# Optimization experiments

Measured on AMD Instinct MI355X. Metric: run time of the kernel, lower is better.

## Reference

```python
import jax, jax.numpy as jnp
import numpy as np

N, D = 8192, 128
BATCH_SIZE = 8192  # init kwarg; final loss divisor
EPS = 1e-12        # F.normalize eps


def _normalize(x):
    n = jnp.maximum(jnp.linalg.norm(x, axis=-1, keepdims=True), EPS)
    return x / n


def _alignment(x, y, alpha=2.0):
    # (x - y).norm(p=2, dim=1).pow(2).mean() == mean of squared row diffs
    return jnp.mean(jnp.sum((x - y) ** 2, axis=1))


def _uniformity(x, t=2.0):
    # torch.pdist(x).pow(2) == squared euclidean distance for all i<j pairs.
    # Use gram-matrix identity; mask to strict upper triangle.
    n = x.shape[0]
    sq = jnp.sum(x * x, axis=1)                      # [N]
    d2 = sq[:, None] + sq[None, :] - 2.0 * (x @ x.T)  # [N, N]
    d2 = jnp.maximum(d2, 0.0)
    iu = jnp.triu(jnp.ones((n, n), dtype=bool), k=1)
    num_pairs = n * (n - 1) // 2
    mean_val = jnp.sum(jnp.where(iu, jnp.exp(-t * d2), 0.0)) / num_pairs
    return jnp.log(mean_val)


def setup_inputs() -> dict:
    key = jax.random.key(0)
    k1, k2, k3 = jax.random.split(key, 3)
    return {
        "users": jax.random.normal(k1, (N, D), dtype=jnp.float32),
        "pos_items": jax.random.normal(k2, (N, D), dtype=jnp.float32),
        "neg_items": jax.random.normal(k3, (N, D), dtype=jnp.float32),
    }


def reference(users, pos_items, neg_items):
    # neg_items is accepted but unused, matching the original forward.
    user_n = _normalize(users)
    item_n = _normalize(pos_items)
    align = _alignment(user_n, item_n)
    uniform = 0.5 * (_uniformity(user_n) + _uniformity(item_n)) / 2.0
    loss = (align + uniform) / BATCH_SIZE
    return loss
```

## Files before the change

### kernel.cpp

```cpp
#include <hip/hip_runtime.h>
#include <hip/hip_bf16.h>

typedef int   i32x4  __attribute__((ext_vector_type(4)));
typedef int   i32x16 __attribute__((ext_vector_type(16)));

#define NROWS 8192
#define DIM   128
#define NB    64
#define JOBS_PER_MAT 2080

__device__ __forceinline__ float waveReduceSum(float v) {
    for (int off = 32; off; off >>= 1) v += __shfl_xor(v, off, 64);
    return v;
}

__device__ __forceinline__ float fast_exp2(float x) {
    return __builtin_amdgcn_exp2f(x);
}

__device__ __forceinline__ void gload16(const void* g, void* l) {
    __builtin_amdgcn_global_load_lds(
        (const __attribute__((address_space(1))) unsigned int*)(uintptr_t)g,
        (__attribute__((address_space(3))) unsigned int*)(uintptr_t)l,
        16, 0, 0);
}

__device__ __forceinline__ int tri(int b) { return b * NB - (b * (b - 1)) / 2; }

__global__ __launch_bounds__(256) void prep_kernel(
    const float* __restrict__ users, const float* __restrict__ pos,
    signed char* __restrict__ U8, signed char* __restrict__ P8,
    double* __restrict__ alignPart)
{
    const int tid  = threadIdx.x;
    const int lane = tid & 63;
    const int w    = tid >> 6;
    const int l32  = lane & 31;
    const int half = lane >> 5;
    const int r    = blockIdx.x * 8 + w * 2 + half;

    const float4 u4 = ((const float4*)users)[r * 32 + l32];
    const float4 p4 = ((const float4*)pos )[r * 32 + l32];

    float su = u4.x*u4.x + u4.y*u4.y + u4.z*u4.z + u4.w*u4.w;
    float sp = p4.x*p4.x + p4.y*p4.y + p4.z*p4.z + p4.w*p4.w;
    for (int off = 16; off; off >>= 1) {
        su += __shfl_xor(su, off, 64);
        sp += __shfl_xor(sp, off, 64);
    }
    const float nu  = fmaxf(sqrtf(su), 1e-12f);
    const float npp = fmaxf(sqrtf(sp), 1e-12f);

    const float ux = u4.x / nu,  uy = u4.y / nu,  uz = u4.z / nu,  uw = u4.w / nu;
    const float px = p4.x / npp, py = p4.y / npp, pz = p4.z / npp, pw = p4.w / npp;

    union { signed char c[4]; int i; } qu, qp;
    qu.c[0] = (signed char)__float2int_rn(ux * 127.0f);
    qu.c[1] = (signed char)__float2int_rn(uy * 127.0f);
    qu.c[2] = (signed char)__float2int_rn(uz * 127.0f);
    qu.c[3] = (signed char)__float2int_rn(uw * 127.0f);
    qp.c[0] = (signed char)__float2int_rn(px * 127.0f);
    qp.c[1] = (signed char)__float2int_rn(py * 127.0f);
    qp.c[2] = (signed char)__float2int_rn(pz * 127.0f);
    qp.c[3] = (signed char)__float2int_rn(pw * 127.0f);
    ((int*)U8)[r * 32 + l32] = qu.i;
    ((int*)P8)[r * 32 + l32] = qp.i;

    const float dx = ux - px, dy = uy - py, dz = uz - pz, dw = uw - pw;
    float al = dx*dx + dy*dy + dz*dz + dw*dw;
    for (int off = 16; off; off >>= 1) al += __shfl_xor(al, off, 64);
    al += __shfl_xor(al, 32, 64);

    __shared__ float wsum[4];
    if (lane == 0) wsum[w] = al;
    __syncthreads();
    if (tid == 0)
        alignPart[blockIdx.x] = (double)wsum[0] + (double)wsum[1]
                              + (double)wsum[2] + (double)wsum[3];
}

__global__ __launch_bounds__(256, 4) void gram_kernel(
    const signed char* __restrict__ U8, const signed char* __restrict__ P8,
    double* __restrict__ Spart)
{
    __shared__ __align__(16) unsigned char smem[32768];
    __shared__ float wsum[4];

    const int bid = blockIdx.x;
    const int mat = bid >= JOBS_PER_MAT;
    const int t   = bid - (mat ? JOBS_PER_MAT : 0);

    int bi = (int)((NB + 0.5f) - sqrtf((NB + 0.5f) * (NB + 0.5f) - 2.0f * (float)t));
    if (bi > 0 && tri(bi) > t) --bi;
    if (tri(bi + 1) <= t) ++bi;
    const int bj = bi + (t - tri(bi));

    const char* __restrict__ Xb = (const char*)(mat ? P8 : U8);

    const int tid  = threadIdx.x;
    const int lane = tid & 63;
    const int w    = tid >> 6;

    const int srow = tid >> 3;
    const int gcOff = (((tid & 7) ^ (srow & 7)) << 4);
    const char* gA0 = Xb + (size_t)(bi * 128 + srow) * 128 + gcOff;
    const char* gB0 = Xb + (size_t)(bj * 128 + srow) * 128 + gcOff;
    unsigned char* lA0 = smem + w * 1024;

#pragma unroll
    for (int i = 0; i < 4; ++i) {
        gload16(gA0 + i * 4096, lA0 + i * 4096);
        gload16(gB0 + i * 4096, lA0 + 16384 + i * 4096);
    }

    const int wm = w >> 1, wn = w & 1;
    const int l32 = lane & 31;
    const int lh  = lane >> 5;
    const unsigned cxor = (unsigned)(l32 & 7);
    const unsigned aRow0 = (unsigned)(wm * 64 + l32);
    const unsigned bRow0 = (unsigned)(wn * 64 + l32);

    i32x16 acc[2][2];
#pragma unroll
    for (int mi = 0; mi < 2; ++mi)
#pragma unroll
        for (int ni = 0; ni < 2; ++ni)
#pragma unroll
            for (int e = 0; e < 16; ++e)
                acc[mi][ni][e] = 0;

    __syncthreads();

#pragma unroll
    for (int ks = 0; ks < 4; ++ks) {
        const unsigned c = (((unsigned)(ks * 2 + lh)) ^ cxor) << 4;
        i32x4 a[2], b[2];
#pragma unroll
        for (int mi = 0; mi < 2; ++mi)
            a[mi] = *reinterpret_cast<const i32x4*>(
                smem + (aRow0 + mi * 32) * 128 + c);
#pragma unroll
        for (int ni = 0; ni < 2; ++ni)
            b[ni] = *reinterpret_cast<const i32x4*>(
                smem + 16384 + (bRow0 + ni * 32) * 128 + c);
#pragma unroll
        for (int mi = 0; mi < 2; ++mi)
#pragma unroll
            for (int ni = 0; ni < 2; ++ni)
                acc[mi][ni] = __builtin_amdgcn_mfma_i32_32x32x32_i8(
                    a[mi], b[ni], acc[mi][ni], 0, 0, 0);
    }

    const float C1  = 4.0f * 1.4426950408889634f;
    const float C1s = C1 / 16129.0f;
    float s0 = 0.f, s1 = 0.f, s2 = 0.f, s3 = 0.f;
#pragma unroll
    for (int mi = 0; mi < 2; ++mi)
#pragma unroll
        for (int ni = 0; ni < 2; ++ni) {
            const i32x16 v = acc[mi][ni];
#pragma unroll
            for (int e = 0; e < 16; e += 4) {
                s0 += fast_exp2(fmaf((float)v[e + 0], C1s, -C1));
                s1 += fast_exp2(fmaf((float)v[e + 1], C1s, -C1));
                s2 += fast_exp2(fmaf((float)v[e + 2], C1s, -C1));
                s3 += fast_exp2(fmaf((float)v[e + 3], C1s, -C1));
            }
        }

    const float s = waveReduceSum((s0 + s1) + (s2 + s3));
    if (lane == 0) wsum[w] = s;
    __syncthreads();
    if (tid == 0) {
        double bs = (double)wsum[0] + (double)wsum[1]
                  + (double)wsum[2] + (double)wsum[3];
        if (bi != bj) bs *= 2.0;
        Spart[bid] = bs;
    }
}

__global__ __launch_bounds__(1024) void finalize_kernel(
    const double* __restrict__ alignPart, const double* __restrict__ Spart,
    float* __restrict__ out)
{
    const int tid = threadIdx.x;
    double a = 0.0, su = 0.0, sp = 0.0;
    for (int i = tid; i < 1024; i += 1024) a += alignPart[i];
    for (int i = tid; i < 2 * JOBS_PER_MAT; i += 1024) {
        const double v = Spart[i];
        if (i < JOBS_PER_MAT) su += v; else sp += v;
    }
    for (int off = 32; off; off >>= 1) {
        a  += __shfl_xor(a,  off, 64);
        su += __shfl_xor(su, off, 64);
        sp += __shfl_xor(sp, off, 64);
    }
    __shared__ double sh[3][16];
    const int lane = tid & 63, wid = tid >> 6;
    if (lane == 0) { sh[0][wid] = a; sh[1][wid] = su; sh[2][wid] = sp; }
    __syncthreads();
    if (tid == 0) {
        double A = 0.0, SU = 0.0, SP = 0.0;
        for (int i = 0; i < 16; ++i) { A += sh[0][i]; SU += sh[1][i]; SP += sh[2][i]; }
        const double Nd = 8192.0;
        const double npairs = Nd * (Nd - 1.0) * 0.5;
        const double align = A / Nd;
        const double mu = (SU - Nd) * 0.5 / npairs;
        const double mp = (SP - Nd) * 0.5 / npairs;
        const double uniform = 0.25 * (log(mu) + log(mp));
        out[0] = (float)((align + uniform) / 8192.0);
    }
}

extern "C" void kernel_launch(void* const* d_in, const int* in_sizes, int n_in,
                              void* d_out, int out_size, void* d_ws, size_t ws_size,
                              hipStream_t stream)
{
    const float* users = (const float*)d_in[0];
    const float* pos   = (const float*)d_in[1];
    float* out = (float*)d_out;

    char* ws = (char*)d_ws;
    signed char* U8 = (signed char*)ws;
    signed char* P8 = (signed char*)(ws + 1048576);
    double* alignPart = (double*)(ws + 2097152);
    double* Spart     = (double*)(ws + 2097152 + 8192);

    hipLaunchKernelGGL(prep_kernel, dim3(1024), dim3(256), 0, stream,
                       users, pos, U8, P8, alignPart);
    hipLaunchKernelGGL(gram_kernel, dim3(2 * JOBS_PER_MAT), dim3(256), 0, stream,
                       U8, P8, Spart);
    hipLaunchKernelGGL(finalize_kernel, dim3(1), dim3(1024), 0, stream,
                       alignPart, Spart, out);
}
```

Before: 33.48 us.

## Process two tile jobs per block with double-buffered K-half pipelining

```diff
diff --git a/kernel.cpp b/kernel.cpp
--- a/kernel.cpp
+++ b/kernel.cpp
@@ -84,16 +84,19 @@
     double* __restrict__ Spart)
 {
     __shared__ __align__(16) unsigned char smem[32768];
-    __shared__ float wsum[4];
-
-    const int bid = blockIdx.x;
-    const int mat = bid >= JOBS_PER_MAT;
-    const int t   = bid - (mat ? JOBS_PER_MAT : 0);
-
-    int bi = (int)((NB + 0.5f) - sqrtf((NB + 0.5f) * (NB + 0.5f) - 2.0f * (float)t));
-    if (bi > 0 && tri(bi) > t) --bi;
-    if (tri(bi + 1) <= t) ++bi;
-    const int bj = bi + (t - tri(bi));
+    __shared__ float wsum[2][4];
+
+    const int blk = blockIdx.x;
+    const int j0  = blk * 2;
+    const int mat = j0 >= JOBS_PER_MAT;
+    const int t0  = j0 - (mat ? JOBS_PER_MAT : 0);
+
+    int bi = (int)((NB + 0.5f) - sqrtf((NB + 0.5f) * (NB + 0.5f) - 2.0f * (float)t0));
+    if (bi > 0 && tri(bi) > t0) --bi;
+    if (tri(bi + 1) <= t0) ++bi;
+    int bj = bi + (t0 - tri(bi));
+    int bi1 = bi, bj1 = bj + 1;
+    if (bj == NB - 1) { bi1 = bi + 1; bj1 = bi1; }
 
     const char* __restrict__ Xb = (const char*)(mat ? P8 : U8);
 
@@ -101,82 +104,119 @@
     const int lane = tid & 63;
     const int w    = tid >> 6;
 
-    const int srow = tid >> 3;
-    const int gcOff = (((tid & 7) ^ (srow & 7)) << 4);
-    const char* gA0 = Xb + (size_t)(bi * 128 + srow) * 128 + gcOff;
-    const char* gB0 = Xb + (size_t)(bj * 128 + srow) * 128 + gcOff;
-    unsigned char* lA0 = smem + w * 1024;
-
-#pragma unroll
-    for (int i = 0; i < 4; ++i) {
-        gload16(gA0 + i * 4096, lA0 + i * 4096);
-        gload16(gB0 + i * 4096, lA0 + 16384 + i * 4096);
+    const int rl = lane >> 2;
+    const int cg = (((lane & 3) ^ (rl & 3)) << 4);
+    unsigned char* lbase = smem + w * 1024;
+
+#define STAGE(p, h, tbi, tbj)                                               \
+    {                                                                       \
+        _Pragma("unroll")                                                   \
+        for (int i_ = 0; i_ < 2; ++i_) {                                    \
+            const int r_ = w * 16 + i_ * 64 + rl;                           \
+            gload16(Xb + (size_t)((tbi) * 128 + r_) * 128 + (h) * 64 + cg,  \
+                    lbase + (p) * 16384 + i_ * 4096);                       \
+            gload16(Xb + (size_t)((tbj) * 128 + r_) * 128 + (h) * 64 + cg,  \
+                    lbase + (p) * 16384 + 8192 + i_ * 4096);                \
+        }                                                                   \
     }
 
     const int wm = w >> 1, wn = w & 1;
     const int l32 = lane & 31;
     const int lh  = lane >> 5;
-    const unsigned cxor = (unsigned)(l32 & 7);
+    const unsigned cxor = (unsigned)(l32 & 3);
     const unsigned aRow0 = (unsigned)(wm * 64 + l32);
     const unsigned bRow0 = (unsigned)(wn * 64 + l32);
 
     i32x16 acc[2][2];
-#pragma unroll
-    for (int mi = 0; mi < 2; ++mi)
-#pragma unroll
-        for (int ni = 0; ni < 2; ++ni)
-#pragma unroll
-            for (int e = 0; e < 16; ++e)
-                acc[mi][ni][e] = 0;
-
-    __syncthreads();
-
-#pragma unroll
-    for (int ks = 0; ks < 4; ++ks) {
-        const unsigned c = (((unsigned)(ks * 2 + lh)) ^ cxor) << 4;
-        i32x4 a[2], b[2];
-#pragma unroll
-        for (int mi = 0; mi < 2; ++mi)
-            a[mi] = *reinterpret_cast<const i32x4*>(
-                smem + (aRow0 + mi * 32) * 128 + c);
-#pragma unroll
-        for (int ni = 0; ni < 2; ++ni)
-            b[ni] = *reinterpret_cast<const i32x4*>(
-                smem + 16384 + (bRow0 + ni * 32) * 128 + c);
-#pragma unroll
-        for (int mi = 0; mi < 2; ++mi)
-#pragma unroll
-            for (int ni = 0; ni < 2; ++ni)
-                acc[mi][ni] = __builtin_amdgcn_mfma_i32_32x32x32_i8(
-                    a[mi], b[ni], acc[mi][ni], 0, 0, 0);
+#define ZEROACC                                                             \
+    _Pragma("unroll")                                                       \
+    for (int mi_ = 0; mi_ < 2; ++mi_)                                       \
+        _Pragma("unroll")                                                   \
+        for (int ni_ = 0; ni_ < 2; ++ni_)                                   \
+            _Pragma("unroll")                                               \
+            for (int e_ = 0; e_ < 16; ++e_)                                 \
+                acc[mi_][ni_][e_] = 0;
+    ZEROACC
+
+#define COMPUTE(p)                                                          \
+    {                                                                       \
+        const unsigned base = (p) * 16384;                                  \
+        _Pragma("unroll")                                                   \
+        for (int ks2 = 0; ks2 < 2; ++ks2) {                                 \
+            const unsigned c = (((unsigned)(ks2 * 2 + lh)) ^ cxor) << 4;    \
+            i32x4 a[2], b[2];                                               \
+            _Pragma("unroll")                                               \
+            for (int mi = 0; mi < 2; ++mi)                                  \
+                a[mi] = *reinterpret_cast<const i32x4*>(                    \
+                    smem + base + (aRow0 + mi * 32) * 64 + c);              \
+            _Pragma("unroll")                                               \
+            for (int ni = 0; ni < 2; ++ni)                                  \
+                b[ni] = *reinterpret_cast<const i32x4*>(                    \
+                    smem + base + 8192 + (bRow0 + ni * 32) * 64 + c);       \
+            _Pragma("unroll")                                               \
+            for (int mi = 0; mi < 2; ++mi)                                  \
+                _Pragma("unroll")                                           \
+                for (int ni = 0; ni < 2; ++ni)                              \
+                    acc[mi][ni] = __builtin_amdgcn_mfma_i32_32x32x32_i8(    \
+                        a[mi], b[ni], acc[mi][ni], 0, 0, 0);                \
+        }                                                                   \
     }
 
     const float C1  = 4.0f * 1.4426950408889634f;
     const float C1s = C1 / 16129.0f;
-    float s0 = 0.f, s1 = 0.f, s2 = 0.f, s3 = 0.f;
-#pragma unroll
-    for (int mi = 0; mi < 2; ++mi)
-#pragma unroll
-        for (int ni = 0; ni < 2; ++ni) {
-            const i32x16 v = acc[mi][ni];
-#pragma unroll
-            for (int e = 0; e < 16; e += 4) {
-                s0 += fast_exp2(fmaf((float)v[e + 0], C1s, -C1));
-                s1 += fast_exp2(fmaf((float)v[e + 1], C1s, -C1));
-                s2 += fast_exp2(fmaf((float)v[e + 2], C1s, -C1));
-                s3 += fast_exp2(fmaf((float)v[e + 3], C1s, -C1));
-            }
-        }
-
-    const float s = waveReduceSum((s0 + s1) + (s2 + s3));
-    if (lane == 0) wsum[w] = s;
-    __syncthreads();
+
+#define EPILOGUE(slot)                                                      \
+    {                                                                       \
+        float s0 = 0.f, s1 = 0.f, s2 = 0.f, s3 = 0.f;                       \
+        _Pragma("unroll")                                                   \
+        for (int mi = 0; mi < 2; ++mi)                                      \
+            _Pragma("unroll")                                               \
+            for (int ni = 0; ni < 2; ++ni) {                                \
+                const i32x16 v = acc[mi][ni];                               \
+                _Pragma("unroll")                                           \
+                for (int e = 0; e < 16; e += 4) {                           \
+                    s0 += fast_exp2(fmaf((float)v[e + 0], C1s, -C1));       \
+                    s1 += fast_exp2(fmaf((float)v[e + 1], C1s, -C1));       \
+                    s2 += fast_exp2(fmaf((float)v[e + 2], C1s, -C1));       \
+                    s3 += fast_exp2(fmaf((float)v[e + 3], C1s, -C1));       \
+                }                                                           \
+            }                                                               \
+        const float s_ = waveReduceSum((s0 + s1) + (s2 + s3));              \
+        if (lane == 0) wsum[slot][w] = s_;                                  \
+    }
+
+    STAGE(0, 0, bi, bj)
+    __syncthreads();
+    STAGE(1, 1, bi, bj)
+    COMPUTE(0)
+    __syncthreads();
+    STAGE(0, 0, bi1, bj1)
+    COMPUTE(1)
+    EPILOGUE(0)
+    ZEROACC
+    __syncthreads();
+    STAGE(1, 1, bi1, bj1)
+    COMPUTE(0)
     if (tid == 0) {
-        double bs = (double)wsum[0] + (double)wsum[1]
-                  + (double)wsum[2] + (double)wsum[3];
+        double bs = (double)wsum[0][0] + (double)wsum[0][1]
+                  + (double)wsum[0][2] + (double)wsum[0][3];
         if (bi != bj) bs *= 2.0;
-        Spart[bid] = bs;
-    }
+        Spart[j0] = bs;
+    }
+    __syncthreads();
+    COMPUTE(1)
+    EPILOGUE(1)
+    __syncthreads();
+    if (tid == 0) {
+        double bs = (double)wsum[1][0] + (double)wsum[1][1]
+                  + (double)wsum[1][2] + (double)wsum[1][3];
+        if (bi1 != bj1) bs *= 2.0;
+        Spart[j0 + 1] = bs;
+    }
+#undef STAGE
+#undef COMPUTE
+#undef ZEROACC
+#undef EPILOGUE
 }
 
 __global__ __launch_bounds__(1024) void finalize_kernel(
@@ -228,7 +268,7 @@
 
     hipLaunchKernelGGL(prep_kernel, dim3(1024), dim3(256), 0, stream,
                        users, pos, U8, P8, alignPart);
-    hipLaunchKernelGGL(gram_kernel, dim3(2 * JOBS_PER_MAT), dim3(256), 0, stream,
+    hipLaunchKernelGGL(gram_kernel, dim3(JOBS_PER_MAT), dim3(256), 0, stream,
                        U8, P8, Spart);
     hipLaunchKernelGGL(finalize_kernel, dim3(1), dim3(1024), 0, stream,
                        alignPart, Spart, out);
```

Result: slower. 35.14 us (+4.9%).

## Give each wave its own 64x64 gram tile loaded directly from global memory

Applied to the files above, without the earlier changes.

```diff
diff --git a/kernel.cpp b/kernel.cpp
--- a/kernel.cpp
+++ b/kernel.cpp
@@ -6,26 +6,14 @@
 
 #define NROWS 8192
 #define DIM   128
-#define NB    64
-#define JOBS_PER_MAT 2080
-
-__device__ __forceinline__ float waveReduceSum(float v) {
-    for (int off = 32; off; off >>= 1) v += __shfl_xor(v, off, 64);
-    return v;
-}
+#define NBW   128
+#define JOBSW 8256
 
 __device__ __forceinline__ float fast_exp2(float x) {
     return __builtin_amdgcn_exp2f(x);
 }
 
-__device__ __forceinline__ void gload16(const void* g, void* l) {
-    __builtin_amdgcn_global_load_lds(
-        (const __attribute__((address_space(1))) unsigned int*)(uintptr_t)g,
-        (__attribute__((address_space(3))) unsigned int*)(uintptr_t)l,
-        16, 0, 0);
-}
-
-__device__ __forceinline__ int tri(int b) { return b * NB - (b * (b - 1)) / 2; }
+__device__ __forceinline__ int tri128(int b) { return b * NBW - (b * (b - 1)) / 2; }
 
 __global__ __launch_bounds__(256) void prep_kernel(
     const float* __restrict__ users, const float* __restrict__ pos,
@@ -79,46 +67,38 @@
                               + (double)wsum[2] + (double)wsum[3];
 }
 
-__global__ __launch_bounds__(256, 4) void gram_kernel(
+__global__ __launch_bounds__(256, 3) void gram_kernel(
     const signed char* __restrict__ U8, const signed char* __restrict__ P8,
     double* __restrict__ Spart)
 {
-    __shared__ __align__(16) unsigned char smem[32768];
-    __shared__ float wsum[4];
-
-    const int bid = blockIdx.x;
-    const int mat = bid >= JOBS_PER_MAT;
-    const int t   = bid - (mat ? JOBS_PER_MAT : 0);
-
-    int bi = (int)((NB + 0.5f) - sqrtf((NB + 0.5f) * (NB + 0.5f) - 2.0f * (float)t));
-    if (bi > 0 && tri(bi) > t) --bi;
-    if (tri(bi + 1) <= t) ++bi;
-    const int bj = bi + (t - tri(bi));
-
-    const char* __restrict__ Xb = (const char*)(mat ? P8 : U8);
-
     const int tid  = threadIdx.x;
     const int lane = tid & 63;
-    const int w    = tid >> 6;
-
-    const int srow = tid >> 3;
-    const int gcOff = (((tid & 7) ^ (srow & 7)) << 4);
-    const char* gA0 = Xb + (size_t)(bi * 128 + srow) * 128 + gcOff;
-    const char* gB0 = Xb + (size_t)(bj * 128 + srow) * 128 + gcOff;
-    unsigned char* lA0 = smem + w * 1024;
-
-#pragma unroll
-    for (int i = 0; i < 4; ++i) {
-        gload16(gA0 + i * 4096, lA0 + i * 4096);
-        gload16(gB0 + i * 4096, lA0 + 16384 + i * 4096);
-    }
-
-    const int wm = w >> 1, wn = w & 1;
+    const int wid  = blockIdx.x * 4 + (tid >> 6);
+
+    const int mat = wid >= JOBSW;
+    const int t   = wid - (mat ? JOBSW : 0);
+
+    int bi = (int)(128.5f - sqrtf(128.5f * 128.5f - 2.0f * (float)t));
+    if (bi > 0 && tri128(bi) > t) --bi;
+    if (tri128(bi + 1) <= t) ++bi;
+    const int bj = bi + (t - tri128(bi));
+
+    const char* __restrict__ Xb = (const char*)(mat ? P8 : U8);
+
     const int l32 = lane & 31;
     const int lh  = lane >> 5;
-    const unsigned cxor = (unsigned)(l32 & 7);
-    const unsigned aRow0 = (unsigned)(wm * 64 + l32);
-    const unsigned bRow0 = (unsigned)(wn * 64 + l32);
+
+    const char* aB = Xb + (size_t)(bi * 64 + l32) * 128 + lh * 16;
+    const char* bB = Xb + (size_t)(bj * 64 + l32) * 128 + lh * 16;
+
+    i32x4 a[2][4], b[2][4];
+#pragma unroll
+    for (int ks = 0; ks < 4; ++ks) {
+        a[0][ks] = *reinterpret_cast<const i32x4*>(aB + ks * 32);
+        a[1][ks] = *reinterpret_cast<const i32x4*>(aB + 32 * 128 + ks * 32);
+        b[0][ks] = *reinterpret_cast<const i32x4*>(bB + ks * 32);
+        b[1][ks] = *reinterpret_cast<const i32x4*>(bB + 32 * 128 + ks * 32);
+    }
 
     i32x16 acc[2][2];
 #pragma unroll
@@ -129,27 +109,14 @@
             for (int e = 0; e < 16; ++e)
                 acc[mi][ni][e] = 0;
 
-    __syncthreads();
-
-#pragma unroll
-    for (int ks = 0; ks < 4; ++ks) {
-        const unsigned c = (((unsigned)(ks * 2 + lh)) ^ cxor) << 4;
-        i32x4 a[2], b[2];
-#pragma unroll
-        for (int mi = 0; mi < 2; ++mi)
-            a[mi] = *reinterpret_cast<const i32x4*>(
-                smem + (aRow0 + mi * 32) * 128 + c);
-#pragma unroll
-        for (int ni = 0; ni < 2; ++ni)
-            b[ni] = *reinterpret_cast<const i32x4*>(
-                smem + 16384 + (bRow0 + ni * 32) * 128 + c);
+#pragma unroll
+    for (int ks = 0; ks < 4; ++ks)
 #pragma unroll
         for (int mi = 0; mi < 2; ++mi)
 #pragma unroll
             for (int ni = 0; ni < 2; ++ni)
                 acc[mi][ni] = __builtin_amdgcn_mfma_i32_32x32x32_i8(
-                    a[mi], b[ni], acc[mi][ni], 0, 0, 0);
-    }
+                    a[mi][ks], b[ni][ks], acc[mi][ni], 0, 0, 0);
 
     const float C1  = 4.0f * 1.4426950408889634f;
     const float C1s = C1 / 16129.0f;
@@ -168,14 +135,13 @@
             }
         }
 
-    const float s = waveReduceSum((s0 + s1) + (s2 + s3));
-    if (lane == 0) wsum[w] = s;
-    __syncthreads();
-    if (tid == 0) {
-        double bs = (double)wsum[0] + (double)wsum[1]
-                  + (double)wsum[2] + (double)wsum[3];
+    float s = (s0 + s1) + (s2 + s3);
+    for (int off = 32; off; off >>= 1) s += __shfl_xor(s, off, 64);
+
+    if (lane == 0) {
+        double bs = (double)s;
         if (bi != bj) bs *= 2.0;
-        Spart[bid] = bs;
+        Spart[wid] = bs;
     }
 }
 
@@ -186,9 +152,9 @@
     const int tid = threadIdx.x;
     double a = 0.0, su = 0.0, sp = 0.0;
     for (int i = tid; i < 1024; i += 1024) a += alignPart[i];
-    for (int i = tid; i < 2 * JOBS_PER_MAT; i += 1024) {
+    for (int i = tid; i < 2 * JOBSW; i += 1024) {
         const double v = Spart[i];
-        if (i < JOBS_PER_MAT) su += v; else sp += v;
+        if (i < JOBSW) su += v; else sp += v;
     }
     for (int off = 32; off; off >>= 1) {
         a  += __shfl_xor(a,  off, 64);
@@ -228,7 +194,7 @@
 
     hipLaunchKernelGGL(prep_kernel, dim3(1024), dim3(256), 0, stream,
                        users, pos, U8, P8, alignPart);
-    hipLaunchKernelGGL(gram_kernel, dim3(2 * JOBS_PER_MAT), dim3(256), 0, stream,
+    hipLaunchKernelGGL(gram_kernel, dim3(2 * JOBSW / 4), dim3(256), 0, stream,
                        U8, P8, Spart);
     hipLaunchKernelGGL(finalize_kernel, dim3(1), dim3(1024), 0, stream,
                        alignPart, Spart, out);
```

New measurement: 50.82 us. 51.8% more time.
